# Optimization experiments

Measured on AMD Instinct MI355X. Metric: run time of the kernel, lower is better.

Reference implementation:

```python
import jax, jax.numpy as jnp
import numpy as np


def setup_inputs() -> dict:
    key = jax.random.key(0)
    ks = jax.random.split(key, 8)
    B, C, H, W = 8, 256, 64, 64
    s = 1.0 / np.sqrt(C)
    return {
        "x": jax.random.normal(ks[0], (B, C, H, W), dtype=jnp.float32),
        "wq": jax.random.normal(ks[1], (C, C), dtype=jnp.float32) * s,
        "bq": jax.random.normal(ks[2], (C,), dtype=jnp.float32) * 0.01,
        "wk": jax.random.normal(ks[3], (C, C), dtype=jnp.float32) * s,
        "bk": jax.random.normal(ks[4], (C,), dtype=jnp.float32) * 0.01,
        "wv": jax.random.normal(ks[5], (C, C), dtype=jnp.float32) * s,
        "bv": jax.random.normal(ks[6], (C,), dtype=jnp.float32) * 0.01,
        "gamma": jax.random.normal(ks[7], (1,), dtype=jnp.float32) * 0.1,
    }


def reference(x, wq, bq, wk, bk, wv, bv, gamma):
    B, C, H, W = x.shape
    N = H * W
    xf = x.reshape(B, C, N)  # flatten spatial -> tokens
    # 1x1 convs == per-pixel linear maps over channels
    q = jnp.einsum('oc,bcn->bon', wq, xf) + bq[None, :, None]  # [B,C,N]
    k = jnp.einsum('oc,bcn->bon', wk, xf) + bk[None, :, None]  # [B,C,N]
    v = jnp.einsum('oc,bcn->bon', wv, xf) + bv[None, :, None]  # [B,C,N]
    # energy[b,n,m] = <q[:, n], k[:, m]>  (query tokens x key tokens)
    energy = jnp.einsum('bcn,bcm->bnm', q, k)  # [B,N,N]
    attention = jax.nn.softmax(energy, axis=-1)
    # out = V @ attention^T : out[b,c,n] = sum_m v[b,c,m] * attention[b,n,m]
    out = jnp.einsum('bcm,bnm->bcn', v, attention).reshape(B, C, H, W)
    return gamma[0] * out + x
```

## Files before the change

kernel.cpp:

```cpp
#include <hip/hip_runtime.h>
#include <hip/hip_bf16.h>
#include <cstdint>


typedef short short8 __attribute__((ext_vector_type(8)));
typedef short short4v __attribute__((ext_vector_type(4)));
typedef float f32x4 __attribute__((ext_vector_type(4)));
typedef unsigned int uint4v __attribute__((ext_vector_type(4)));

#define MFMA16(a, b, c) __builtin_amdgcn_mfma_f32_16x16x32_bf16((a), (b), (c), 0, 0, 0)
#define LOG2E 1.4426950408889634f

__device__ __forceinline__ unsigned short f2bf(float f) {
    union { float f; unsigned int u; } v;
    v.f = f;
    unsigned int u = v.u;
    return (unsigned short)((u + 0x7fffu + ((u >> 16) & 1u)) >> 16);
}

__device__ __forceinline__ void load_lds16(const unsigned short* g, unsigned short* l) {
    __builtin_amdgcn_global_load_lds(
        (const __attribute__((address_space(1))) unsigned int*)g,
        (__attribute__((address_space(3))) unsigned int*)l, 16, 0, 0);
}

__device__ __forceinline__ float rowmax16_dpp(float x) {
    int v;
    v = __builtin_amdgcn_update_dpp(0, __float_as_int(x), 0x121, 0xf, 0xf, false);
    x = fmaxf(x, __int_as_float(v));
    v = __builtin_amdgcn_update_dpp(0, __float_as_int(x), 0x122, 0xf, 0xf, false);
    x = fmaxf(x, __int_as_float(v));
    v = __builtin_amdgcn_update_dpp(0, __float_as_int(x), 0x124, 0xf, 0xf, false);
    x = fmaxf(x, __int_as_float(v));
    v = __builtin_amdgcn_update_dpp(0, __float_as_int(x), 0x128, 0xf, 0xf, false);
    x = fmaxf(x, __int_as_float(v));
    return x;
}

__device__ __forceinline__ float wavemax_bcast(float x) {
    int v;
    v = __builtin_amdgcn_update_dpp(__float_as_int(x), __float_as_int(x), 0x142, 0xf, 0xf, false);
    x = fmaxf(x, __int_as_float(v));
    v = __builtin_amdgcn_update_dpp(__float_as_int(x), __float_as_int(x), 0x143, 0xf, 0xf, false);
    x = fmaxf(x, __int_as_float(v));
    return __int_as_float(__builtin_amdgcn_readlane(__float_as_int(x), 63));
}

__global__ __launch_bounds__(256) void wcvt_kernel(
    const float* __restrict__ wq, const float* __restrict__ wk,
    const float* __restrict__ wv, unsigned short* __restrict__ Wb)
{
    int idx = (blockIdx.x * 256 + threadIdx.x) * 4;
    const float* src = (idx < 65536) ? wq : ((idx < 131072) ? wk : wv);
    float4 f = *(const float4*)(src + (idx & 65535));
    short4v s = { (short)f2bf(f.x), (short)f2bf(f.y), (short)f2bf(f.z), (short)f2bf(f.w) };
    *(short4v*)(Wb + idx) = s;
}

__global__ __launch_bounds__(256, 2) void qkv_kernel(
    const float* __restrict__ x, const unsigned short* __restrict__ Wb,
    const float* __restrict__ bq, const float* __restrict__ bk,
    const float* __restrict__ bv,
    unsigned short* __restrict__ Qc, unsigned short* __restrict__ Kr,
    unsigned short* __restrict__ Vc)
{
    const int C = 256, N = 4096;
    __shared__ __align__(16) unsigned short Xt[32][264];

    const int tid  = threadIdx.x;
    const int bid  = blockIdx.x;
    const int b    = bid >> 7;
    const int n0   = (bid & 127) * 32;
    const int wave = tid >> 6;
    const int lane = tid & 63;
    const int quad = lane >> 4;
    const int l16  = lane & 15;
    const int ch0  = wave * 64;

    {
        const int token = tid & 31;
        const int cg    = tid >> 5;
        const float* xb = x + ((size_t)b * C) * N + n0 + token;
#pragma unroll
        for (int p = 0; p < 8; p++) {
            int c0 = p * 32 + cg * 4;
            float f0 = xb[(size_t)(c0 + 0) * N];
            float f1 = xb[(size_t)(c0 + 1) * N];
            float f2 = xb[(size_t)(c0 + 2) * N];
            float f3 = xb[(size_t)(c0 + 3) * N];
            short4v s = { (short)f2bf(f0), (short)f2bf(f1), (short)f2bf(f2), (short)f2bf(f3) };
            *(short4v*)(&Xt[token][c0]) = s;
        }
    }
    __syncthreads();

    f32x4 acc[4][2];

#pragma unroll
    for (int ct = 0; ct < 4; ct++)
#pragma unroll
        for (int tt = 0; tt < 2; tt++) acc[ct][tt] = (f32x4){0.f, 0.f, 0.f, 0.f};
#pragma unroll
    for (int kc = 0; kc < 8; kc++) {
        const int ko = kc * 32 + quad * 8;
        short8 ax0 = *(const short8*)(&Xt[l16][ko]);
        short8 ax1 = *(const short8*)(&Xt[16 + l16][ko]);
#pragma unroll
        for (int ct = 0; ct < 4; ct++) {
            short8 wf = *(const short8*)(Wb + (ch0 + ct * 16 + l16) * 256 + ko);
            acc[ct][0] = MFMA16(ax0, wf, acc[ct][0]);
            acc[ct][1] = MFMA16(ax1, wf, acc[ct][1]);
        }
    }
#pragma unroll
    for (int ct = 0; ct < 4; ct++) {
        const int ch = ch0 + ct * 16 + l16;
        const float biq = bq[ch];
        uint4v qv;
#pragma unroll
        for (int r = 0; r < 4; r++) {
            unsigned int lo = f2bf((acc[ct][0][r] + biq) * LOG2E);
            unsigned int hi = f2bf((acc[ct][1][r] + biq) * LOG2E);
            qv[r] = lo | (hi << 16);
        }
        *(uint4v*)(Qc + ((size_t)b * C + ch) * N + n0 + quad * 8) = qv;
    }

#pragma unroll
    for (int ct = 0; ct < 4; ct++)
#pragma unroll
        for (int tt = 0; tt < 2; tt++) acc[ct][tt] = (f32x4){0.f, 0.f, 0.f, 0.f};
#pragma unroll
    for (int kc = 0; kc < 8; kc++) {
        const int ko = kc * 32 + quad * 8;
        short8 ax0 = *(const short8*)(&Xt[l16][ko]);
        short8 ax1 = *(const short8*)(&Xt[16 + l16][ko]);
#pragma unroll
        for (int ct = 0; ct < 4; ct++) {
            short8 wf = *(const short8*)(Wb + (2 << 16) + (ch0 + ct * 16 + l16) * 256 + ko);
            acc[ct][0] = MFMA16(ax0, wf, acc[ct][0]);
            acc[ct][1] = MFMA16(ax1, wf, acc[ct][1]);
        }
    }
#pragma unroll
    for (int ct = 0; ct < 4; ct++) {
        const int ch = ch0 + ct * 16 + l16;
        const float biv = bv[ch];
        uint4v vv;
#pragma unroll
        for (int r = 0; r < 4; r++) {
            unsigned int lo = f2bf(acc[ct][0][r] + biv);
            unsigned int hi = f2bf(acc[ct][1][r] + biv);
            vv[r] = lo | (hi << 16);
        }
        *(uint4v*)(Vc + ((size_t)b * C + ch) * N + n0 + quad * 8) = vv;
    }

#pragma unroll
    for (int ct = 0; ct < 4; ct++)
#pragma unroll
        for (int tt = 0; tt < 2; tt++) acc[ct][tt] = (f32x4){0.f, 0.f, 0.f, 0.f};
#pragma unroll
    for (int kc = 0; kc < 8; kc++) {
        const int ko = kc * 32 + quad * 8;
        short8 ax0 = *(const short8*)(&Xt[l16][ko]);
        short8 ax1 = *(const short8*)(&Xt[16 + l16][ko]);
#pragma unroll
        for (int ct = 0; ct < 4; ct++) {
            short8 wf = *(const short8*)(Wb + (1 << 16) + (ch0 + ct * 16 + l16) * 256 + ko);
            acc[ct][0] = MFMA16(ax0, wf, acc[ct][0]);
            acc[ct][1] = MFMA16(ax1, wf, acc[ct][1]);
        }
    }
    __syncthreads();
#pragma unroll
    for (int ct = 0; ct < 4; ct++) {
        const int ch = ch0 + ct * 16 + l16;
        const float bik = bk[ch];
#pragma unroll
        for (int tt = 0; tt < 2; tt++) {
#pragma unroll
            for (int r = 0; r < 4; r++)
                Xt[tt * 16 + quad * 4 + r][ch] = f2bf(acc[ct][tt][r] + bik);
        }
    }
    __syncthreads();
#pragma unroll
    for (int p = 0; p < 2; p++) {
        int chunk = p * 256 + tid;
        int tok = chunk >> 4;
        int cc  = (chunk & 15) * 16;
        *(short8*)(Kr + ((size_t)b * N + n0 + tok) * C + cc) = *(const short8*)(&Xt[tok][cc]);
    }
}

__global__ __launch_bounds__(512, 2) void attn_kernel(
    const unsigned short* __restrict__ Qc,
    const unsigned short* __restrict__ Kr,
    const unsigned short* __restrict__ Vc,
    const float* __restrict__ x,
    const float* __restrict__ gamma,
    float* __restrict__ out)
{
    const int C = 256, N = 4096;
    __shared__ __align__(16) unsigned short KV[2][32768];
    __shared__ float Lw[8][32];
    __shared__ float MwL[4];

    const int tid  = threadIdx.x;
    const int wave = tid >> 6;
    const int ks   = wave >> 2;
    const int w4   = wave & 3;
    const int lane = tid & 63;
    const int quad = lane >> 4;
    const int l16  = lane & 15;
    const int bid  = blockIdx.x;
    const int b    = bid & 7;
    const int q0   = (bid >> 3) * 128 + w4 * 32;

    const unsigned short* kb  = Kr + (size_t)b * N * C;
    const unsigned short* vcb = Vc + (size_t)b * C * N;

    short8 aqL[8], aqH[8];
    {
        const unsigned int* qb32 = (const unsigned int*)(Qc + (size_t)b * C * N);
#pragma unroll
        for (int f = 0; f < 8; f++) {
#pragma unroll
            for (int j = 0; j < 8; j++) {
                size_t i32 = ((size_t)(f * 32 + quad * 8 + j) * N + q0) / 2 + l16;
                unsigned int u = qb32[i32];
                aqL[f][j] = (short)(u & 0xffff);
                aqH[f][j] = (short)(u >> 16);
            }
        }
    }

    f32x4 oL[16], oH[16];
#pragma unroll
    for (int t = 0; t < 16; t++) {
        oL[t] = (f32x4){0.f, 0.f, 0.f, 0.f};
        oH[t] = (f32x4){0.f, 0.f, 0.f, 0.f};
    }
    float m_w = -__builtin_inff();
    float l_pL = 0.f, l_pH = 0.f;

    auto stage = [&](int buf, int m0) {
        unsigned short* dst = &KV[buf][0];
#pragma unroll
        for (int p = 0; p < 4; p++) {
            int chunk = p * 512 + tid;
            int half = chunk >> 10;
            int idx  = chunk & 1023;
            int key = idx >> 5;
            int j = (idx & 31) ^ (key & 31);
            load_lds16(kb + (size_t)(half * 2048 + m0 + key) * C + j * 8,
                       dst + half * 16384 + idx * 8);
        }
#pragma unroll
        for (int p = 0; p < 4; p++) {
            int chunk = p * 512 + tid;
            int half = chunk >> 10;
            int idx  = chunk & 1023;
            int c = idx >> 2;
            int j = (idx & 3) ^ (c & 3);
            load_lds16(vcb + (size_t)c * N + half * 2048 + m0 + j * 8,
                       dst + half * 16384 + 8192 + idx * 8);
        }
    };

    stage(0, 0);
    __syncthreads();

    for (int it = 0; it < 64; ++it) {
        const int cur = it & 1;
        if (it < 63) stage(cur ^ 1, (it + 1) * 32);

        const unsigned short* Kb = &KV[cur][ks * 16384];
        const unsigned short* Vb = Kb + 8192;

        f32x4 tL0 = {0.f,0.f,0.f,0.f}, tL1 = {0.f,0.f,0.f,0.f};
        f32x4 tH0 = {0.f,0.f,0.f,0.f}, tH1 = {0.f,0.f,0.f,0.f};
#pragma unroll
        for (int f = 0; f < 8; f++) {
            const int j = f * 4 + quad;
            int k0 = l16, k1 = 16 + l16;
            short8 kf0 = *(const short8*)(Kb + (k0 * 32 + (j ^ (k0 & 31))) * 8);
            short8 kf1 = *(const short8*)(Kb + (k1 * 32 + (j ^ (k1 & 31))) * 8);
            tL0 = MFMA16(kf0, aqL[f], tL0);
            tL1 = MFMA16(kf1, aqL[f], tL1);
            tH0 = MFMA16(kf0, aqH[f], tH0);
            tH1 = MFMA16(kf1, aqH[f], tH1);
        }

        float mx = fmaxf(fmaxf(fmaxf(tL0[0], tL0[1]), fmaxf(tL0[2], tL0[3])),
                         fmaxf(fmaxf(tL1[0], tL1[1]), fmaxf(tL1[2], tL1[3])));
        mx = fmaxf(mx, fmaxf(fmaxf(fmaxf(tH0[0], tH0[1]), fmaxf(tH0[2], tH0[3])),
                             fmaxf(fmaxf(tH1[0], tH1[1]), fmaxf(tH1[2], tH1[3]))));
        mx = rowmax16_dpp(mx);
        mx = wavemax_bcast(mx);

        if (mx > m_w + 8.0f) {
            const float al = exp2f(m_w - mx);
            m_w = mx;
            l_pL *= al; l_pH *= al;
#pragma unroll
            for (int t = 0; t < 16; t++) { oL[t] *= al; oH[t] *= al; }
        }
        const float mn = m_w;

        uint4v apLu, apHu;
#pragma unroll
        for (int w = 0; w < 4; w++) {
            float e0 = exp2f(tL0[w] - mn);
            float e1 = exp2f(tL1[w] - mn);
            l_pL += e0 + e1;
            union { __hip_bfloat162 v; unsigned int u; } cv;
            cv.v = __float22bfloat162_rn(float2{e0, e1});
            apLu[w] = cv.u;
            float g0 = exp2f(tH0[w] - mn);
            float g1 = exp2f(tH1[w] - mn);
            l_pH += g0 + g1;
            union { __hip_bfloat162 v; unsigned int u; } cw;
            cw.v = __float22bfloat162_rn(float2{g0, g1});
            apHu[w] = cw.u;
        }
        short8 apL, apH;
        {
            union { uint4v u; short8 s; } c1; c1.u = apLu; apL = c1.s;
            union { uint4v u; short8 s; } c2; c2.u = apHu; apH = c2.s;
        }

#pragma unroll
        for (int t = 0; t < 16; t++) {
            int c = t * 16 + l16;
            short8 vf = *(const short8*)(Vb + (c * 4 + (quad ^ (c & 3))) * 8);
            oL[t] = MFMA16(apL, vf, oL[t]);
            oH[t] = MFMA16(apH, vf, oH[t]);
        }
        __syncthreads();
    }

    l_pL += __shfl_xor(l_pL, 16);
    l_pL += __shfl_xor(l_pL, 32);
    l_pH += __shfl_xor(l_pH, 16);
    l_pH += __shfl_xor(l_pH, 32);
    if (quad == 0) {
        Lw[wave][l16] = l_pL;
        Lw[wave][16 + l16] = l_pH;
    }

    float* CombF = (float*)(&KV[0][0]);
    __syncthreads();
    if (ks == 1) {
#pragma unroll
        for (int t = 0; t < 16; t++) {
#pragma unroll
            for (int r = 0; r < 4; r++) {
                CombF[(size_t)(w4 * 32 + quad * 4 + r) * 256 + t * 16 + l16] = oL[t][r];
                CombF[(size_t)(w4 * 32 + 16 + quad * 4 + r) * 256 + t * 16 + l16] = oH[t][r];
            }
        }
        if (lane == 0) MwL[w4] = m_w;
    }
    __syncthreads();
    if (ks == 0) {
        const float g = gamma[0];
        const float m2w = MwL[w4];
        const float mt = fmaxf(m_w, m2w);
        const float f1 = exp2f(m_w - mt);
        const float f2 = exp2f(m2w - mt);
        float linv[2][4];
#pragma unroll
        for (int h = 0; h < 2; h++)
#pragma unroll
            for (int r = 0; r < 4; r++) {
                const int q = h * 16 + quad * 4 + r;
                linv[h][r] = g / (Lw[w4][q] * f1 + Lw[4 + w4][q] * f2);
            }
#pragma unroll
        for (int t = 0; t < 16; t++) {
            const int c = t * 16 + l16;
#pragma unroll
            for (int h = 0; h < 2; h++) {
                const int nb = q0 + h * 16 + quad * 4;
                f32x4 o1 = h ? oH[t] : oL[t];
                f32x4 ov;
#pragma unroll
                for (int r = 0; r < 4; r++) {
                    float o2 = CombF[(size_t)(w4 * 32 + h * 16 + quad * 4 + r) * 256 + c];
                    ov[r] = (o1[r] * f1 + o2 * f2) * linv[h][r];
                }
                size_t idx = ((size_t)(b * C + c)) * N + nb;
                f32x4 xv = *(const f32x4*)(x + idx);
                *(f32x4*)(out + idx) = ov + xv;
            }
        }
    }
}

extern "C" void kernel_launch(void* const* d_in, const int* in_sizes, int n_in,
                              void* d_out, int out_size, void* d_ws, size_t ws_size,
                              hipStream_t stream) {
    const int B = 8, C = 256, N = 4096;
    const float* x     = (const float*)d_in[0];
    const float* wq    = (const float*)d_in[1];
    const float* bq    = (const float*)d_in[2];
    const float* wk    = (const float*)d_in[3];
    const float* bk    = (const float*)d_in[4];
    const float* wv    = (const float*)d_in[5];
    const float* bv    = (const float*)d_in[6];
    const float* gamma = (const float*)d_in[7];
    float* out = (float*)d_out;

    unsigned short* Qc = (unsigned short*)d_ws;
    unsigned short* Kr = Qc + (size_t)B * C * N;
    unsigned short* Vc = Kr + (size_t)B * N * C;
    unsigned short* Wb = Vc + (size_t)B * C * N;

    wcvt_kernel<<<dim3(192), 256, 0, stream>>>(wq, wk, wv, Wb);
    qkv_kernel<<<dim3(1024), 256, 0, stream>>>(x, Wb, bq, bk, bv, Qc, Kr, Vc);
    attn_kernel<<<dim3(256), 512, 0, stream>>>(Qc, Kr, Vc, x, gamma, out);
}
```

Measured before the change: 367.6 us.

## Drop split-KV within attention block; use 4 waves over full key range

The attention kernel no longer splits the key range across two wave groups with a cross-group softmax merge through LDS. Each block now runs 256 threads (4 waves), and each wave loops over all 128 key tiles alone, which removes the combine step and halves the LDS footprint per block. The V tile swizzle is also rewritten as a rotation so the per-lane LDS read offset is a precomputed constant. In exchange, each block has half as many waves to hide latency, and the serial loop per wave is twice as long.

Result: slower. 493.7 us (+34.3%).

```diff
diff --git a/kernel.cpp b/kernel.cpp
--- a/kernel.cpp
+++ b/kernel.cpp
@@ -194,7 +194,7 @@
     }
 }
 
-__global__ __launch_bounds__(512, 2) void attn_kernel(
+__global__ __launch_bounds__(256, 2) void attn_kernel(
     const unsigned short* __restrict__ Qc,
     const unsigned short* __restrict__ Kr,
     const unsigned short* __restrict__ Vc,
@@ -203,20 +203,17 @@
     float* __restrict__ out)
 {
     const int C = 256, N = 4096;
-    __shared__ __align__(16) unsigned short KV[2][32768];
-    __shared__ float Lw[8][32];
-    __shared__ float MwL[4];
+    __shared__ __align__(16) unsigned short KV[2][16384];
+    __shared__ float Lw[4][32];
 
     const int tid  = threadIdx.x;
     const int wave = tid >> 6;
-    const int ks   = wave >> 2;
-    const int w4   = wave & 3;
     const int lane = tid & 63;
     const int quad = lane >> 4;
     const int l16  = lane & 15;
     const int bid  = blockIdx.x;
     const int b    = bid & 7;
-    const int q0   = (bid >> 3) * 128 + w4 * 32;
+    const int q0   = (bid >> 3) * 128 + wave * 32;
 
     const unsigned short* kb  = Kr + (size_t)b * N * C;
     const unsigned short* vcb = Vc + (size_t)b * C * N;
@@ -249,34 +246,31 @@
         unsigned short* dst = &KV[buf][0];
 #pragma unroll
         for (int p = 0; p < 4; p++) {
-            int chunk = p * 512 + tid;
-            int half = chunk >> 10;
-            int idx  = chunk & 1023;
+            int idx = p * 256 + tid;
             int key = idx >> 5;
             int j = (idx & 31) ^ (key & 31);
-            load_lds16(kb + (size_t)(half * 2048 + m0 + key) * C + j * 8,
-                       dst + half * 16384 + idx * 8);
+            load_lds16(kb + (size_t)(m0 + key) * C + j * 8, dst + idx * 8);
         }
 #pragma unroll
         for (int p = 0; p < 4; p++) {
-            int chunk = p * 512 + tid;
-            int half = chunk >> 10;
-            int idx  = chunk & 1023;
+            int idx = p * 256 + tid;
             int c = idx >> 2;
-            int j = (idx & 3) ^ (c & 3);
-            load_lds16(vcb + (size_t)c * N + half * 2048 + m0 + j * 8,
-                       dst + half * 16384 + 8192 + idx * 8);
+            int s = idx & 3;
+            int j = (s - (c >> 1)) & 3;
+            load_lds16(vcb + (size_t)c * N + m0 + j * 8, dst + 8192 + idx * 8);
         }
     };
 
     stage(0, 0);
     __syncthreads();
 
-    for (int it = 0; it < 64; ++it) {
+    const int vsl = ((quad + (l16 >> 1)) & 3) * 8;
+
+    for (int it = 0; it < 128; ++it) {
         const int cur = it & 1;
-        if (it < 63) stage(cur ^ 1, (it + 1) * 32);
-
-        const unsigned short* Kb = &KV[cur][ks * 16384];
+        if (it < 127) stage(cur ^ 1, (it + 1) * 32);
+
+        const unsigned short* Kb = &KV[cur][0];
         const unsigned short* Vb = Kb + 8192;
 
         f32x4 tL0 = {0.f,0.f,0.f,0.f}, tL1 = {0.f,0.f,0.f,0.f};
@@ -333,8 +327,7 @@
 
 #pragma unroll
         for (int t = 0; t < 16; t++) {
-            int c = t * 16 + l16;
-            short8 vf = *(const short8*)(Vb + (c * 4 + (quad ^ (c & 3))) * 8);
+            short8 vf = *(const short8*)(Vb + t * 512 + l16 * 32 + vsl);
             oL[t] = MFMA16(apL, vf, oL[t]);
             oH[t] = MFMA16(apH, vf, oH[t]);
         }
@@ -349,35 +342,16 @@
         Lw[wave][l16] = l_pL;
         Lw[wave][16 + l16] = l_pH;
     }
-
-    float* CombF = (float*)(&KV[0][0]);
-    __syncthreads();
-    if (ks == 1) {
-#pragma unroll
-        for (int t = 0; t < 16; t++) {
-#pragma unroll
-            for (int r = 0; r < 4; r++) {
-                CombF[(size_t)(w4 * 32 + quad * 4 + r) * 256 + t * 16 + l16] = oL[t][r];
-                CombF[(size_t)(w4 * 32 + 16 + quad * 4 + r) * 256 + t * 16 + l16] = oH[t][r];
-            }
-        }
-        if (lane == 0) MwL[w4] = m_w;
-    }
-    __syncthreads();
-    if (ks == 0) {
+    __syncthreads();
+
+    {
         const float g = gamma[0];
-        const float m2w = MwL[w4];
-        const float mt = fmaxf(m_w, m2w);
-        const float f1 = exp2f(m_w - mt);
-        const float f2 = exp2f(m2w - mt);
         float linv[2][4];
 #pragma unroll
         for (int h = 0; h < 2; h++)
 #pragma unroll
-            for (int r = 0; r < 4; r++) {
-                const int q = h * 16 + quad * 4 + r;
-                linv[h][r] = g / (Lw[w4][q] * f1 + Lw[4 + w4][q] * f2);
-            }
+            for (int r = 0; r < 4; r++)
+                linv[h][r] = g / Lw[wave][h * 16 + quad * 4 + r];
 #pragma unroll
         for (int t = 0; t < 16; t++) {
             const int c = t * 16 + l16;
@@ -387,10 +361,7 @@
                 f32x4 o1 = h ? oH[t] : oL[t];
                 f32x4 ov;
 #pragma unroll
-                for (int r = 0; r < 4; r++) {
-                    float o2 = CombF[(size_t)(w4 * 32 + h * 16 + quad * 4 + r) * 256 + c];
-                    ov[r] = (o1[r] * f1 + o2 * f2) * linv[h][r];
-                }
+                for (int r = 0; r < 4; r++) ov[r] = o1[r] * linv[h][r];
                 size_t idx = ((size_t)(b * C + c)) * N + nb;
                 f32x4 xv = *(const f32x4*)(x + idx);
                 *(f32x4*)(out + idx) = ov + xv;
@@ -420,5 +391,5 @@
 
     wcvt_kernel<<<dim3(192), 256, 0, stream>>>(wq, wk, wv, Wb);
     qkv_kernel<<<dim3(1024), 256, 0, stream>>>(x, Wb, bq, bk, bv, Qc, Kr, Vc);
-    attn_kernel<<<dim3(256), 512, 0, stream>>>(Qc, Kr, Vc, x, gamma, out);
-}
+    attn_kernel<<<dim3(256), 256, 0, stream>>>(Qc, Kr, Vc, x, gamma, out);
+}
```

## Software-pipeline QK of next tile with softmax and PV of current tile

Applied to the files above, without the earlier changes.

Restructures the attention loop so the QK^T MFMAs for the next KV tile are issued before the PV MFMAs of the current tile. This lets the matrix-core work overlap the softmax's exp/max latency. The next-next tile's load is now issued after the PV step, and an extra barrier is added per iteration. The V LDS swizzle also changes to a rotation pattern with a precomputed per-lane offset, which simplifies addressing and is meant to avoid bank conflicts. The cost is higher register pressure from keeping QK results live across the iteration.

After: 362.5 us. No clear change (-1.4%).

```diff
diff --git a/kernel.cpp b/kernel.cpp
--- a/kernel.cpp
+++ b/kernel.cpp
@@ -263,36 +263,41 @@
             int half = chunk >> 10;
             int idx  = chunk & 1023;
             int c = idx >> 2;
-            int j = (idx & 3) ^ (c & 3);
+            int s = idx & 3;
+            int j = (s - (c >> 1)) & 3;
             load_lds16(vcb + (size_t)c * N + half * 2048 + m0 + j * 8,
                        dst + half * 16384 + 8192 + idx * 8);
         }
     };
 
-    stage(0, 0);
-    __syncthreads();
-
-    for (int it = 0; it < 64; ++it) {
-        const int cur = it & 1;
-        if (it < 63) stage(cur ^ 1, (it + 1) * 32);
-
-        const unsigned short* Kb = &KV[cur][ks * 16384];
-        const unsigned short* Vb = Kb + 8192;
-
-        f32x4 tL0 = {0.f,0.f,0.f,0.f}, tL1 = {0.f,0.f,0.f,0.f};
-        f32x4 tH0 = {0.f,0.f,0.f,0.f}, tH1 = {0.f,0.f,0.f,0.f};
+    f32x4 tL0, tL1, tH0, tH1;
+
+    auto qk = [&](int buf) {
+        const unsigned short* Kb = &KV[buf][ks * 16384];
+        f32x4 a0 = {0.f,0.f,0.f,0.f}, a1 = {0.f,0.f,0.f,0.f};
+        f32x4 b0 = {0.f,0.f,0.f,0.f}, b1 = {0.f,0.f,0.f,0.f};
 #pragma unroll
         for (int f = 0; f < 8; f++) {
             const int j = f * 4 + quad;
             int k0 = l16, k1 = 16 + l16;
             short8 kf0 = *(const short8*)(Kb + (k0 * 32 + (j ^ (k0 & 31))) * 8);
             short8 kf1 = *(const short8*)(Kb + (k1 * 32 + (j ^ (k1 & 31))) * 8);
-            tL0 = MFMA16(kf0, aqL[f], tL0);
-            tL1 = MFMA16(kf1, aqL[f], tL1);
-            tH0 = MFMA16(kf0, aqH[f], tH0);
-            tH1 = MFMA16(kf1, aqH[f], tH1);
-        }
-
+            a0 = MFMA16(kf0, aqL[f], a0);
+            a1 = MFMA16(kf1, aqL[f], a1);
+            b0 = MFMA16(kf0, aqH[f], b0);
+            b1 = MFMA16(kf1, aqH[f], b1);
+        }
+        tL0 = a0; tL1 = a1; tH0 = b0; tH1 = b1;
+    };
+
+    const int vsl = ((quad + (l16 >> 1)) & 3) * 8;
+
+    stage(0, 0);
+    __syncthreads();
+    stage(1, 32);
+    qk(0);
+
+    for (int it = 0; it < 64; ++it) {
         float mx = fmaxf(fmaxf(fmaxf(tL0[0], tL0[1]), fmaxf(tL0[2], tL0[3])),
                          fmaxf(fmaxf(tL1[0], tL1[1]), fmaxf(tL1[2], tL1[3])));
         mx = fmaxf(mx, fmaxf(fmaxf(fmaxf(tH0[0], tH0[1]), fmaxf(tH0[2], tH0[3])),
@@ -331,14 +336,22 @@
             union { uint4v u; short8 s; } c2; c2.u = apHu; apH = c2.s;
         }
 
-#pragma unroll
-        for (int t = 0; t < 16; t++) {
-            int c = t * 16 + l16;
-            short8 vf = *(const short8*)(Vb + (c * 4 + (quad ^ (c & 3))) * 8);
-            oL[t] = MFMA16(apL, vf, oL[t]);
-            oH[t] = MFMA16(apH, vf, oH[t]);
+        if (it < 63) {
+            __syncthreads();
+            qk((it + 1) & 1);
+        }
+
+        {
+            const unsigned short* Vb = &KV[it & 1][ks * 16384 + 8192];
+#pragma unroll
+            for (int t = 0; t < 16; t++) {
+                short8 vf = *(const short8*)(Vb + t * 512 + l16 * 32 + vsl);
+                oL[t] = MFMA16(apL, vf, oL[t]);
+                oH[t] = MFMA16(apH, vf, oH[t]);
+            }
         }
         __syncthreads();
+        if (it < 62) stage(it & 1, (it + 2) * 32);
     }
 
     l_pL += __shfl_xor(l_pL, 16);
```
